# Kernel tuning notes

Hardware: AMD Instinct MI355X
Metric: run time of the kernel (lower is better)

## Reference

```python
import jax, jax.numpy as jnp
import numpy as np

# ---- static config (from init_kwargs) ----
B_, L_, DM = 4, 2048, 1024
EXPAND, HEADDIM, DSTATE, DCONV = 2, 64, 64, 7
DIN = EXPAND * DM            # 2048
NH = DIN // HEADDIM          # 32
CONV_DIM = DIN + 2 * DSTATE  # 2176 (x, B, C go through the depthwise conv)
DPROJ = 2 * DIN + 2 * DSTATE + 2 * NH  # 4288 (z, xBC, dt_fwd, dt_bwd)
EPS = 1e-5


def setup_inputs() -> dict:
    key = jax.random.key(0)
    ks = jax.random.split(key, 8)
    s = lambda d: 1.0 / np.sqrt(d)
    # dt_bias = inv_softplus(dt) with dt ~ logUniform(1e-3, 0.1)  (Mamba2/Hydra init)
    dt = jnp.exp(jax.random.uniform(ks[3], (NH,)) * (np.log(0.1) - np.log(0.001)) + np.log(0.001))
    return {
        "x": jax.random.normal(ks[0], (B_, L_, DM), jnp.float32),
        "ln_gamma": jnp.ones((DM,), jnp.float32),
        "ln_beta": jnp.zeros((DM,), jnp.float32),
        "W_in": jax.random.normal(ks[1], (DPROJ, DM), jnp.float32) * s(DM),
        "conv_w": jax.random.normal(ks[2], (CONV_DIM, DCONV), jnp.float32) * s(DCONV),
        "conv_b": jnp.zeros((CONV_DIM,), jnp.float32),
        "dt_bias": jnp.log(jnp.expm1(dt)),
        "A_log": jnp.log(jax.random.uniform(ks[4], (NH,), minval=1.0, maxval=16.0)),
        "fc_D_w": jax.random.normal(ks[5], (NH, DIN), jnp.float32) * s(DIN),
        "D": jnp.ones((NH,), jnp.float32),
        "norm_w": jnp.ones((DIN,), jnp.float32),
        "W_out": jax.random.normal(ks[6], (DM, DIN), jnp.float32) * s(DIN),
    }


def _hydra_layer(x, ln_gamma, ln_beta, W_in, conv_w, conv_b, dt_bias, A_log,
                 fc_D_w, D, norm_w, W_out):
    res = x
    # LayerNorm
    mu = jnp.mean(x, -1, keepdims=True)
    var = jnp.mean((x - mu) ** 2, -1, keepdims=True)
    u = (x - mu) * jax.lax.rsqrt(var + EPS) * ln_gamma + ln_beta

    # input projection -> z (gate), xBC (conv stream), dt (fwd+bwd)
    zxbcdt = jnp.einsum('bld,pd->blp', u, W_in)
    z = zxbcdt[..., :DIN]
    xBC = zxbcdt[..., DIN:DIN + CONV_DIM]
    dt = zxbcdt[..., DIN + CONV_DIM:]               # (B,L,2*NH)

    # depthwise 'same' conv along L + SiLU (bidirectional model -> symmetric pad)
    xBC_c = jax.lax.conv_general_dilated(
        xBC.transpose(0, 2, 1), conv_w[:, None, :], (1,),
        [(DCONV // 2, DCONV // 2)], feature_group_count=CONV_DIM)
    xBC = jax.nn.silu((xBC_c + conv_b[None, :, None]).transpose(0, 2, 1))

    xs = xBC[..., :DIN]                             # (B,L,DIN)
    Bm = xBC[..., DIN:DIN + DSTATE]                 # (B,L,N)
    Cm = xBC[..., DIN + DSTATE:]                    # (B,L,N)

    flip = lambda a: a[:, ::-1]
    # stack forward and (flipped) backward direction along batch
    dt2 = jax.nn.softplus(jnp.concatenate([dt[..., :NH], flip(dt[..., NH:])], 0) + dt_bias)  # (2B,L,NH)
    x2 = jnp.concatenate([xs, flip(xs)], 0).reshape(2 * B_, L_, NH, HEADDIM)
    B2 = jnp.concatenate([Bm, flip(Bm)], 0)
    C2 = jnp.concatenate([Cm, flip(Cm)], 0)

    A = -jnp.exp(A_log)                             # (NH,)
    dA = jnp.exp(dt2 * A)                           # (2B,L,NH)

    # selective SSM recurrence: h_t = dA_t * h_{t-1} + dt_t * x_t B_t^T ; y_t = h_t C_t
    def step(h, inp):
        dA_t, dt_t, B_t, C_t, x_t = inp
        dBx = (dt_t[:, :, None, None] * x_t[..., None]) * B_t[:, None, None, :]
        h = dA_t[:, :, None, None] * h + dBx        # (2B,NH,P,N)
        y = jnp.einsum('bhpn,bn->bhp', h, C_t)
        return h, y

    h0 = jnp.zeros((2 * B_, NH, HEADDIM, DSTATE), x.dtype)
    tr = lambda a: jnp.moveaxis(a, 1, 0)
    _, ys = jax.lax.scan(step, h0, (tr(dA), tr(dt2), tr(B2), tr(C2), tr(x2)))
    y = jnp.moveaxis(ys, 0, 1)                      # (2B,L,NH,P)

    # shift by one: strictly off-diagonal part of the quasiseparable mixing matrix
    y = jnp.concatenate([jnp.zeros_like(y[:, :1]), y[:, :-1]], axis=1)
    y = y[:B_] + flip(y[B_:])                       # (B,L,NH,P)

    # data-dependent diagonal: D(x) = fc_D(x) + D, applied per head
    Ddata = jnp.einsum('bld,hd->blh', xs, fc_D_w) + D
    y = y + xs.reshape(B_, L_, NH, HEADDIM) * Ddata[..., None]
    y = y.reshape(B_, L_, DIN)

    # gated RMSNorm (norm after gate)
    y = y * jax.nn.silu(z)
    y = y * jax.lax.rsqrt(jnp.mean(y * y, -1, keepdims=True) + EPS) * norm_w

    # out proj + residual (dropout is identity in eval)
    return res + jnp.einsum('bli,di->bld', y, W_out)


def reference(x, ln_gamma, ln_beta, W_in, conv_w, conv_b, dt_bias, A_log,
              fc_D_w, D, norm_w, W_out):
    return _hydra_layer(x, ln_gamma, ln_beta, W_in, conv_w, conv_b, dt_bias,
                        A_log, fc_D_w, D, norm_w, W_out)
```

## Files before the change

kernel.cpp:

```cpp
#include <hip/hip_runtime.h>
#include <stdint.h>

#define B_   4
#define L_   2048
#define DM   1024
#define DIN  2048
#define NH   32
#define HD   64
#define DSTATE 64
#define DCONV  7
#define CONV_DIM 2176
#define DPROJ 4288
#define NPAD 4352
#define BL   8192
#define EPS  1e-5f
#define QC   128
#define NCH  16

typedef unsigned short u16;
typedef unsigned int   u32;
typedef __bf16 bf16x8 __attribute__((ext_vector_type(8)));
typedef float  f32x4  __attribute__((ext_vector_type(4)));

__device__ __forceinline__ float b2f(u32 b) { return __uint_as_float(b << 16); }
__device__ __forceinline__ u16 f2b(float f) {
    u32 u = __float_as_uint(f);
    u32 r = (u + 0x7fffu + ((u >> 16) & 1u)) >> 16;
    return (u16)r;
}
__device__ __forceinline__ void unpack8(uint4 v, float* f) {
    f[0] = b2f(v.x & 0xffffu); f[1] = b2f(v.x >> 16);
    f[2] = b2f(v.y & 0xffffu); f[3] = b2f(v.y >> 16);
    f[4] = b2f(v.z & 0xffffu); f[5] = b2f(v.z >> 16);
    f[6] = b2f(v.w & 0xffffu); f[7] = b2f(v.w >> 16);
}
__device__ __forceinline__ uint4 pack8(const float* f) {
    uint4 v;
    v.x = (u32)f2b(f[0]) | ((u32)f2b(f[1]) << 16);
    v.y = (u32)f2b(f[2]) | ((u32)f2b(f[3]) << 16);
    v.z = (u32)f2b(f[4]) | ((u32)f2b(f[5]) << 16);
    v.w = (u32)f2b(f[6]) | ((u32)f2b(f[7]) << 16);
    return v;
}
__device__ __forceinline__ int xts(int p, int s) { return p * 136 + ((p >> 3) << 3) + s; }
__device__ __forceinline__ void gload_lds16(const u16* g, u16* l) {
    __builtin_amdgcn_global_load_lds((const __attribute__((address_space(1))) void*)g,
                                     (__attribute__((address_space(3))) void*)l, 16, 0, 0);
}

__global__ __launch_bounds__(256) void k_cvt_win(const float* __restrict__ W, u16* __restrict__ Wb) {
    int idx = blockIdx.x * 256 + threadIdx.x;
    int n = idx >> 10;
    float v = (n < DPROJ) ? W[(size_t)n * DM + (idx & 1023)] : 0.f;
    Wb[idx] = f2b(v);
}
__global__ __launch_bounds__(256) void k_cvt_wout(const float* __restrict__ W, u16* __restrict__ Wb) {
    int idx = blockIdx.x * 256 + threadIdx.x;
    Wb[idx] = f2b(W[idx]);
}
__global__ __launch_bounds__(256) void k_cvt_fcd(const float* __restrict__ W, u16* __restrict__ Wb) {
    int idx = blockIdx.x * 256 + threadIdx.x;
    Wb[idx] = f2b(W[idx]);
}

__global__ __launch_bounds__(256) void k_ln(const float* __restrict__ x, const float* __restrict__ g,
                                            const float* __restrict__ be, u16* __restrict__ u) {
    int row = blockIdx.x, tid = threadIdx.x;
    const float4* xr = (const float4*)(x + (size_t)row * DM);
    float4 v = xr[tid];
    float s1 = v.x + v.y + v.z + v.w;
    float s2 = v.x * v.x + v.y * v.y + v.z * v.z + v.w * v.w;
    for (int o = 32; o; o >>= 1) { s1 += __shfl_down(s1, o); s2 += __shfl_down(s2, o); }
    __shared__ float ls1[4], ls2[4];
    int w = tid >> 6;
    if ((tid & 63) == 0) { ls1[w] = s1; ls2[w] = s2; }
    __syncthreads();
    float t1 = ls1[0] + ls1[1] + ls1[2] + ls1[3];
    float t2 = ls2[0] + ls2[1] + ls2[2] + ls2[3];
    float mu = t1 * (1.f / DM);
    float var = t2 * (1.f / DM) - mu * mu;
    float rs = rsqrtf(var + EPS);
    float4 gv = ((const float4*)g)[tid];
    float4 bv = ((const float4*)be)[tid];
    float o0 = (v.x - mu) * rs * gv.x + bv.x;
    float o1 = (v.y - mu) * rs * gv.y + bv.y;
    float o2 = (v.z - mu) * rs * gv.z + bv.z;
    float o3 = (v.w - mu) * rs * gv.w + bv.w;
    uint2 p;
    p.x = (u32)f2b(o0) | ((u32)f2b(o1) << 16);
    p.y = (u32)f2b(o2) | ((u32)f2b(o3) << 16);
    ((uint2*)(u + (size_t)row * DM))[tid] = p;
}

#define G3_DSA(d, kh, ms)                                                        \
  { _Pragma("unroll")                                                            \
    for (int mi = 0; mi < 4; mi++)                                               \
      af_[mi] = *(const bf16x8*)&Asl[d][kh][a_rd + (ms) * 2048 + mi * 512]; }
#define G3_DSB(d, kh)                                                            \
  { _Pragma("unroll")                                                            \
    for (int nj = 0; nj < 4; nj++)                                               \
      bf_[nj] = *(const bf16x8*)&Bsl[d][kh][b_rd + nj * 512]; }
#define G3_STA(d, kh, tau)                                                       \
  { const size_t ko = (size_t)((tau) * 64 + (kh) * 32);                          \
    gload_lds16(Ag + a_src + ko, &Asl[d][kh][st_l]);                             \
    gload_lds16(Ag + a_src + srowK + ko, &Asl[d][kh][st_l + 512]); }
#define G3_STB(d, kh, tau)                                                       \
  { const size_t ko = (size_t)((tau) * 64 + (kh) * 32);                          \
    gload_lds16(Bg + b_src + ko, &Bsl[d][kh][st_l]);                             \
    gload_lds16(Bg + b_src + srowK + ko, &Bsl[d][kh][st_l + 512]); }
#define G3_MM(ms)                                                                \
  { __builtin_amdgcn_s_barrier();                                                \
    asm volatile("s_waitcnt lgkmcnt(0)" ::: "memory");                           \
    __builtin_amdgcn_sched_barrier(0);                                           \
    __builtin_amdgcn_s_setprio(1);                                               \
    _Pragma("unroll")                                                            \
    for (int mi = 0; mi < 4; mi++)                                               \
      _Pragma("unroll")                                                          \
      for (int nj = 0; nj < 4; nj++)                                             \
        acc[ms][mi][nj] = __builtin_amdgcn_mfma_f32_16x16x32_bf16(af_[mi], bf_[nj], acc[ms][mi][nj], 0, 0, 0); \
    __builtin_amdgcn_s_setprio(0);                                               \
    asm volatile("" ::: "memory");                                               \
    __builtin_amdgcn_s_barrier(); }
#define G3_VM4 asm volatile("s_waitcnt vmcnt(4)" ::: "memory");
#define G3_VM0 asm volatile("s_waitcnt vmcnt(0)" ::: "memory");

__global__ __launch_bounds__(512, 2) void k_gemm256(const u16* __restrict__ Ag, const u16* __restrict__ Bg,
                                                    int K, u16* __restrict__ obf, int ldo) {
    __shared__ __align__(16) u16 Asl[2][2][8192];
    __shared__ __align__(16) u16 Bsl[2][2][8192];
    const int tid = threadIdx.x;
    const int w = tid >> 6, lane = tid & 63, lr = lane & 15, lq = lane >> 4;
    const int wm = w >> 2, wn = w & 3;
    const int bid = blockIdx.x;
    const int swz = (bid & 7) * 68 + (bid >> 3);
    const int bx = swz >> 5, by = swz & 31;
    const int m0 = by * 256, n0 = bx * 256;
    const int sr = lane >> 2;
    const int sc = (lane & 3) ^ ((lane >> 3) & 3);
    const size_t a_src = (size_t)(m0 + w * 32 + sr) * K + sc * 8;
    const size_t b_src = (size_t)(n0 + w * 32 + sr) * K + sc * 8;
    const size_t srowK = (size_t)16 * K;
    const int st_l = w * 1024;
    const int swc = (lq ^ ((lr >> 1) & 3)) << 3;
    const int a_rd = (wm * 128 + lr) * 32 + swc;
    const int b_rd = (wn * 64 + lr) * 32 + swc;

    f32x4 acc[2][4][4];
    #pragma unroll
    for (int s = 0; s < 2; s++)
        #pragma unroll
        for (int i = 0; i < 4; i++)
            #pragma unroll
            for (int j = 0; j < 4; j++) acc[s][i][j] = (f32x4){0.f, 0.f, 0.f, 0.f};

    bf16x8 af_[4], bf_[4];

    G3_STA(0, 0, 0); G3_STB(0, 0, 0);
    G3_STA(0, 1, 0); G3_STB(0, 1, 0);
    G3_STA(1, 0, 1); G3_STB(1, 0, 1);
    G3_VM0;
    __builtin_amdgcn_s_barrier();

    const int NI = K >> 7;
    for (int i = 0; i < NI - 1; ++i) {
        const int t = 2 * i;
        G3_DSB(0, 0) G3_DSA(0, 0, 0) G3_STA(1, 1, t + 1);          G3_MM(0)
        G3_DSA(0, 0, 1) G3_STB(1, 1, t + 1); G3_VM4;               G3_MM(1)
        G3_DSB(0, 1) G3_DSA(0, 1, 0) G3_STA(0, 0, t + 2);          G3_MM(0)
        G3_DSA(0, 1, 1) G3_STB(0, 0, t + 2);                       G3_MM(1)
        G3_DSB(1, 0) G3_DSA(1, 0, 0) G3_STA(0, 1, t + 2);          G3_MM(0)
        G3_DSA(1, 0, 1) G3_STB(0, 1, t + 2); G3_VM4;               G3_MM(1)
        G3_DSB(1, 1) G3_DSA(1, 1, 0) G3_STA(1, 0, t + 3);          G3_MM(0)
        G3_DSA(1, 1, 1) G3_STB(1, 0, t + 3);                       G3_MM(1)
    }
    {
        const int t = 2 * (NI - 1);
        G3_DSB(0, 0) G3_DSA(0, 0, 0) G3_STA(1, 1, t + 1);          G3_MM(0)
        G3_DSA(0, 0, 1) G3_STB(1, 1, t + 1); G3_VM4;               G3_MM(1)
        G3_DSB(0, 1) G3_DSA(0, 1, 0)                               G3_MM(0)
        G3_DSA(0, 1, 1)                                            G3_MM(1)
        G3_DSB(1, 0) G3_DSA(1, 0, 0)                               G3_MM(0)
        G3_DSA(1, 0, 1) G3_VM0;                                    G3_MM(1)
        G3_DSB(1, 1) G3_DSA(1, 1, 0)                               G3_MM(0)
        G3_DSA(1, 1, 1)                                            G3_MM(1)
    }

    #pragma unroll
    for (int ms = 0; ms < 2; ms++)
        #pragma unroll
        for (int mi = 0; mi < 4; mi++)
            #pragma unroll
            for (int nj = 0; nj < 4; nj++)
                #pragma unroll
                for (int rr = 0; rr < 4; rr++) {
                    int m = m0 + wm * 128 + ms * 64 + mi * 16 + lq * 4 + rr;
                    int n = n0 + wn * 64 + nj * 16 + lr;
                    obf[(size_t)m * ldo + n] = f2b(acc[ms][mi][nj][rr]);
                }
}

__global__ __launch_bounds__(256) void k_gemm_bt(const u16* __restrict__ A, const u16* __restrict__ Bw,
                                                 int M, int N, int K, int out_bf16,
                                                 u16* __restrict__ obf, int ldo,
                                                 float* __restrict__ ofp, const float* __restrict__ res) {
    __shared__ __align__(16) u16 As[128 * 64];
    __shared__ __align__(16) u16 Bs[128 * 64];
    int tid = threadIdx.x;
    int m0 = blockIdx.y * 128, n0 = blockIdx.x * 128;
    int w = tid >> 6, lane = tid & 63;
    int wm = (w >> 1) * 64, wn = (w & 1) * 64;
    int lr = lane & 15, lq = lane >> 4;

    f32x4 acc[4][4];
    #pragma unroll
    for (int i = 0; i < 4; i++)
        #pragma unroll
        for (int j = 0; j < 4; j++) acc[i][j] = (f32x4){0.f, 0.f, 0.f, 0.f};

    for (int kt = 0; kt < K; kt += 64) {
        #pragma unroll
        for (int it = 0; it < 4; it++) {
            int s_idx = it * 256 + tid;
            int row = s_idx >> 3;
            int kcg = (s_idx & 7) ^ (row & 7);
            u16* lbase_a = &As[(it * 256 + w * 64) * 8];
            u16* lbase_b = &Bs[(it * 256 + w * 64) * 8];
            gload_lds16(A + (size_t)(m0 + row) * K + kt + kcg * 8, lbase_a);
            gload_lds16(Bw + (size_t)(n0 + row) * K + kt + kcg * 8, lbase_b);
        }
        __syncthreads();
        #pragma unroll
        for (int kk = 0; kk < 2; kk++) {
            bf16x8 af[4], bfr[4];
            #pragma unroll
            for (int i = 0; i < 4; i++) {
                int row = wm + 16 * i + lr;
                af[i] = *(const bf16x8*)&As[row * 64 + (((kk * 4 + lq)) ^ (row & 7)) * 8];
            }
            #pragma unroll
            for (int j = 0; j < 4; j++) {
                int row = wn + 16 * j + lr;
                bfr[j] = *(const bf16x8*)&Bs[row * 64 + (((kk * 4 + lq)) ^ (row & 7)) * 8];
            }
            #pragma unroll
            for (int i = 0; i < 4; i++)
                #pragma unroll
                for (int j = 0; j < 4; j++)
                    acc[i][j] = __builtin_amdgcn_mfma_f32_16x16x32_bf16(af[i], bfr[j], acc[i][j], 0, 0, 0);
        }
        __syncthreads();
    }
    #pragma unroll
    for (int i = 0; i < 4; i++) {
        #pragma unroll
        for (int j = 0; j < 4; j++) {
            #pragma unroll
            for (int rr = 0; rr < 4; rr++) {
                int m = m0 + wm + 16 * i + lq * 4 + rr;
                int n = n0 + wn + 16 * j + lr;
                float v = acc[i][j][rr];
                if (out_bf16) obf[(size_t)m * ldo + n] = f2b(v);
                else          ofp[(size_t)m * ldo + n] = v + res[(size_t)m * ldo + n];
            }
        }
    }
}

__global__ __launch_bounds__(256) void k_dproj(const u16* __restrict__ xs, const u16* __restrict__ fcb,
                                               const float* __restrict__ Dv, float* __restrict__ Dd) {
    __shared__ __align__(16) u16 As[32 * 72];
    __shared__ __align__(16) u16 Bs[32 * 72];
    int tid = threadIdx.x;
    int m0 = blockIdx.x * 32;
    int w = tid >> 6, lane = tid & 63, lr = lane & 15, lq = lane >> 4;
    int mt = (w & 1) * 16, nt = (w >> 1) * 16;
    int r = tid >> 3, kc = tid & 7;
    f32x4 acc = (f32x4){0.f, 0.f, 0.f, 0.f};
    for (int kt = 0; kt < DIN; kt += 64) {
        *(uint4*)&As[r * 72 + kc * 8] = *(const uint4*)(xs + (size_t)(m0 + r) * DIN + kt + kc * 8);
        *(uint4*)&Bs[r * 72 + kc * 8] = *(const uint4*)(fcb + (size_t)r * DIN + kt + kc * 8);
        __syncthreads();
        #pragma unroll
        for (int ks = 0; ks < 2; ks++) {
            bf16x8 a = *(const bf16x8*)&As[(mt + lr) * 72 + ks * 32 + lq * 8];
            bf16x8 b = *(const bf16x8*)&Bs[(nt + lr) * 72 + ks * 32 + lq * 8];
            acc = __builtin_amdgcn_mfma_f32_16x16x32_bf16(a, b, acc, 0, 0, 0);
        }
        __syncthreads();
    }
    #pragma unroll
    for (int rr = 0; rr < 4; rr++) {
        int m = m0 + mt + lq * 4 + rr;
        int n = nt + lr;
        Dd[(size_t)m * 32 + n] = acc[rr] + Dv[n];
    }
}

__global__ __launch_bounds__(256) void k_conv(const u16* __restrict__ zx, const float* __restrict__ cw,
                                              const float* __restrict__ cb, u16* __restrict__ xs,
                                              u16* __restrict__ BCb) {
    __shared__ u16 sh[262 * 64];
    int c0 = blockIdx.x * 64, t0 = blockIdx.y * 256, b = blockIdx.z;
    int tid = threadIdx.x;
    int c = tid & 63, tg = tid >> 6;
    for (int it = 0; it < 66; it++) {
        int r = it * 4 + tg;
        if (r < 262) {
            int t = t0 + r - 3;
            u16 v = 0;
            if (t >= 0 && t < L_) v = zx[(size_t)(b * L_ + t) * NPAD + DIN + c0 + c];
            sh[r * 64 + c] = v;
        }
    }
    float wgt[7];
    #pragma unroll
    for (int k = 0; k < 7; k++) wgt[k] = cw[(c0 + c) * 7 + k];
    float bias = cb[c0 + c];
    __syncthreads();
    int cg = c0 + c;
    for (int tt = 0; tt < 64; tt++) {
        int tl = tt * 4 + tg;
        float a = bias;
        #pragma unroll
        for (int k = 0; k < 7; k++) a += b2f(sh[(tl + k) * 64 + c]) * wgt[k];
        float v = a / (1.f + __expf(-a));
        size_t row = (size_t)b * L_ + (t0 + tl);
        if (cg < DIN) xs[row * DIN + cg] = f2b(v);
        else          BCb[row * 128 + (cg - DIN)] = f2b(v);
    }
}

__global__ __launch_bounds__(256) void k_chunk(const u16* __restrict__ xs, const u16* __restrict__ BCb,
                                               const u16* __restrict__ zx, const float* __restrict__ dt_bias,
                                               const float* __restrict__ A_log, u16* __restrict__ y0,
                                               u16* __restrict__ y1, float* __restrict__ wout,
                                               float* __restrict__ decay, u16* __restrict__ scb) {
    __shared__ __align__(16) u16 ab[18432];
    __shared__ __align__(16) u16 XT[8768];
    __shared__ __align__(16) u16 BT[8768];
    __shared__ __align__(16) float dts_s[128];
    __shared__ __align__(16) float lda_s[128];
    __shared__ __align__(16) float wend[128];
    __shared__ __align__(16) double cumd[128];

    const int blk = blockIdx.x;
    const int c = blk & 15, dbh = blk >> 4;
    const int h = dbh & 31, b = (dbh >> 5) & 3, dir = dbh >> 7;
    const int tid = threadIdx.x, w = tid >> 6, lane = tid & 63, lr = lane & 15, lq = lane >> 4;
    const int s0 = c * QC;
    u16* yo = dir ? y1 : y0;

    if (tid < 128) {
        int s = s0 + tid;
        int t = dir ? (L_ - 1 - s) : s;
        float draw = b2f(zx[(size_t)(b * L_ + t) * NPAD + (DIN + CONV_DIM) + dir * 32 + h]);
        float xb = draw + dt_bias[h];
        float dt2 = (xb > 20.f) ? xb : log1pf(__expf(xb));
        dts_s[tid] = dt2;
        lda_s[tid] = -__expf(A_log[h]) * dt2;
    }
    {
        int sl0 = tid >> 3, ng = (tid & 7) * 8;
        #pragma unroll
        for (int it = 0; it < 4; it++) {
            int sl = sl0 + it * 32;
            int s = s0 + sl;
            int t = dir ? (L_ - 1 - s) : s;
            size_t row = (size_t)b * L_ + t;
            const u16* bcr = BCb + row * 128;
            uint4 cv = *(const uint4*)(bcr + 64 + ng);
            *(uint4*)&ab[sl * 72 + ng] = cv;
            uint4 pb = *(const uint4*)(bcr + ng);
            *(uint4*)&ab[9216 + sl * 72 + ng] = pb;
            u16 bh[8] = {(u16)(pb.x & 0xffffu), (u16)(pb.x >> 16), (u16)(pb.y & 0xffffu), (u16)(pb.y >> 16),
                         (u16)(pb.z & 0xffffu), (u16)(pb.z >> 16), (u16)(pb.w & 0xffffu), (u16)(pb.w >> 16)};
            #pragma unroll
            for (int i = 0; i < 8; i++) BT[(ng + i) * 136 + ng + sl] = bh[i];
            uint4 xv = *(const uint4*)(xs + row * DIN + h * 64 + ng);
            u16 xh[8] = {(u16)(xv.x & 0xffffu), (u16)(xv.x >> 16), (u16)(xv.y & 0xffffu), (u16)(xv.y >> 16),
                         (u16)(xv.z & 0xffffu), (u16)(xv.z >> 16), (u16)(xv.w & 0xffffu), (u16)(xv.w >> 16)};
            #pragma unroll
            for (int i = 0; i < 8; i++) XT[(ng + i) * 136 + ng + sl] = xh[i];
        }
    }
    __syncthreads();
    if (w == 0) {
        double v0 = (double)lda_s[lane];
        double v1 = (double)lda_s[64 + lane];
        #pragma unroll
        for (int o = 1; o < 64; o <<= 1) {
            double t0 = __shfl_up(v0, o);
            double t1 = __shfl_up(v1, o);
            if (lane >= o) { v0 += t0; v1 += t1; }
        }
        double tot0 = __shfl(v0, 63);
        cumd[lane] = v0;
        cumd[64 + lane] = tot0 + v1;
    }
    bf16x8 af[2][2];
    #pragma unroll
    for (int ti = 0; ti < 2; ti++)
        #pragma unroll
        for (int ks = 0; ks < 2; ks++)
            af[ti][ks] = *(const bf16x8*)&ab[(w * 32 + ti * 16 + lr) * 72 + ks * 32 + lq * 8];
    f32x4 accg[2][8];
    #pragma unroll
    for (int ti = 0; ti < 2; ti++)
        #pragma unroll
        for (int si = 0; si < 8; si++) accg[ti][si] = (f32x4){0.f, 0.f, 0.f, 0.f};
    #pragma unroll
    for (int si = 0; si < 8; si++)
        #pragma unroll
        for (int ks = 0; ks < 2; ks++) {
            bf16x8 bf = *(const bf16x8*)&ab[9216 + (si * 16 + lr) * 72 + ks * 32 + lq * 8];
            accg[0][si] = __builtin_amdgcn_mfma_f32_16x16x32_bf16(af[0][ks], bf, accg[0][si], 0, 0, 0);
            accg[1][si] = __builtin_amdgcn_mfma_f32_16x16x32_bf16(af[1][ks], bf, accg[1][si], 0, 0, 0);
        }
    __syncthreads();
    if (tid < 128) wend[tid] = __expf((float)(cumd[127] - cumd[tid])) * dts_s[tid];
    {
        double cumt_d[8];
        #pragma unroll
        for (int ti = 0; ti < 2; ti++)
            #pragma unroll
            for (int r = 0; r < 4; r++) cumt_d[ti * 4 + r] = cumd[w * 32 + ti * 16 + lq * 4 + r];
        double cums_d[8]; float dts_l[8];
        #pragma unroll
        for (int si = 0; si < 8; si++) { cums_d[si] = cumd[si * 16 + lr]; dts_l[si] = dts_s[si * 16 + lr]; }
        #pragma unroll
        for (int ti = 0; ti < 2; ti++)
            #pragma unroll
            for (int si = 0; si < 8; si++)
                #pragma unroll
                for (int r = 0; r < 4; r++) {
                    int t_l = w * 32 + ti * 16 + lq * 4 + r;
                    int s_l = si * 16 + lr;
                    float v = 0.f;
                    if (s_l <= t_l)
                        v = __expf((float)(cumt_d[ti * 4 + r] - cums_d[si])) * dts_l[si] * accg[ti][si][r];
                    ab[xts(t_l, s_l)] = f2b(v);
                }
    }
    __syncthreads();
    f32x4 acc[2][4];
    #pragma unroll
    for (int ti = 0; ti < 2; ti++)
        #pragma unroll
        for (int pj = 0; pj < 4; pj++) acc[ti][pj] = (f32x4){0.f, 0.f, 0.f, 0.f};
    #pragma unroll
    for (int ks = 0; ks < 4; ks++) {
        bf16x8 a0 = *(const bf16x8*)&ab[xts(w * 32 + lr, ks * 32 + lq * 8)];
        bf16x8 a1 = *(const bf16x8*)&ab[xts(w * 32 + 16 + lr, ks * 32 + lq * 8)];
        #pragma unroll
        for (int pj = 0; pj < 4; pj++) {
            bf16x8 bf = *(const bf16x8*)&XT[xts(pj * 16 + lr, ks * 32 + lq * 8)];
            acc[0][pj] = __builtin_amdgcn_mfma_f32_16x16x32_bf16(a0, bf, acc[0][pj], 0, 0, 0);
            acc[1][pj] = __builtin_amdgcn_mfma_f32_16x16x32_bf16(a1, bf, acc[1][pj], 0, 0, 0);
        }
    }
    #pragma unroll
    for (int ti = 0; ti < 2; ti++)
        #pragma unroll
        for (int pj = 0; pj < 4; pj++)
            #pragma unroll
            for (int r = 0; r < 4; r++) {
                int t_l = w * 32 + ti * 16 + lq * 4 + r;
                int s = s0 + t_l;
                int t = dir ? (L_ - 1 - s) : s;
                yo[((size_t)b * L_ + t) * DIN + h * 64 + pj * 16 + lr] = f2b(acc[ti][pj][r]);
            }
    f32x4 accs[4];
    #pragma unroll
    for (int nj = 0; nj < 4; nj++) accs[nj] = (f32x4){0.f, 0.f, 0.f, 0.f};
    #pragma unroll
    for (int ks = 0; ks < 4; ks++) {
        uint4 xv = *(const uint4*)&XT[xts(w * 16 + lr, ks * 32 + lq * 8)];
        float xf[8]; unpack8(xv, xf);
        float4 w0 = *(const float4*)&wend[ks * 32 + lq * 8];
        float4 w1 = *(const float4*)&wend[ks * 32 + lq * 8 + 4];
        float fs[8] = {xf[0]*w0.x, xf[1]*w0.y, xf[2]*w0.z, xf[3]*w0.w,
                       xf[4]*w1.x, xf[5]*w1.y, xf[6]*w1.z, xf[7]*w1.w};
        bf16x8 a = __builtin_bit_cast(bf16x8, pack8(fs));
        #pragma unroll
        for (int nj = 0; nj < 4; nj++) {
            bf16x8 bb = *(const bf16x8*)&BT[xts(nj * 16 + lr, ks * 32 + lq * 8)];
            accs[nj] = __builtin_amdgcn_mfma_f32_16x16x32_bf16(a, bb, accs[nj], 0, 0, 0);
        }
    }
    #pragma unroll
    for (int nj = 0; nj < 4; nj++)
        #pragma unroll
        for (int r = 0; r < 4; r++) {
            int p = w * 16 + lq * 4 + r, n = nj * 16 + lr;
            scb[(size_t)blk * 4096 + p * 64 + n] = f2b(accs[nj][r]);
        }
    if (tid < 128) wout[dbh * 2048 + s0 + tid] = __expf((float)cumd[tid]);
    if (tid == 0)  decay[blk] = __expf((float)cumd[127]);
}

__global__ __launch_bounds__(256) void k_hscan(const float* __restrict__ decay, u16* __restrict__ scb) {
    int dbh = blockIdx.x, tid = threadIdx.x;
    u16* base = scb + (size_t)dbh * 16 * 4096 + tid * 16;
    float hcur[16];
    #pragma unroll
    for (int i = 0; i < 16; i++) hcur[i] = 0.f;
    for (int c = 0; c < NCH; c++) {
        u16* sg = base + (size_t)c * 4096;
        uint4 q0 = *(const uint4*)sg;
        uint4 q1 = *(const uint4*)(sg + 8);
        float sf[16]; unpack8(q0, sf); unpack8(q1, sf + 8);
        *(uint4*)sg       = pack8(hcur);
        *(uint4*)(sg + 8) = pack8(hcur + 8);
        float dk = decay[dbh * 16 + c];
        #pragma unroll
        for (int i = 0; i < 16; i++) hcur[i] = dk * hcur[i] + sf[i];
    }
}

__global__ __launch_bounds__(256) void k_inter(const u16* __restrict__ BCb, const float* __restrict__ wout,
                                               const u16* __restrict__ hin, u16* __restrict__ y0,
                                               u16* __restrict__ y1) {
    __shared__ __align__(16) u16 Csc[128 * 72];
    __shared__ __align__(16) u16 hs[64 * 72];
    const int blk = blockIdx.x;
    const int c = blk & 15, dbh = blk >> 4;
    const int h = dbh & 31, b = (dbh >> 5) & 3, dir = dbh >> 7;
    const int tid = threadIdx.x, w = tid >> 6, lane = tid & 63, lr = lane & 15, lq = lane >> 4;
    u16* yo = dir ? y1 : y0;

    {
        int g = tid * 16, p = g >> 6, n = g & 63;
        const u16* hg = hin + (size_t)blk * 4096 + g;
        *(uint4*)&hs[p * 72 + n]     = *(const uint4*)hg;
        *(uint4*)&hs[p * 72 + n + 8] = *(const uint4*)(hg + 8);
    }
    const int sl0 = tid >> 3, ng = (tid & 7) * 8;
    #pragma unroll
    for (int it = 0; it < 4; it++) {
        int sl = sl0 + it * 32;
        int s = c * QC + sl;
        int t = dir ? (L_ - 1 - s) : s;
        const u16* bcr = BCb + ((size_t)b * L_ + t) * 128 + 64 + ng;
        float sc = wout[dbh * 2048 + s];
        uint4 cv = *(const uint4*)bcr;
        float cf[8]; unpack8(cv, cf);
        float f[8] = {cf[0]*sc, cf[1]*sc, cf[2]*sc, cf[3]*sc, cf[4]*sc, cf[5]*sc, cf[6]*sc, cf[7]*sc};
        *(uint4*)&Csc[sl * 72 + ng] = pack8(f);
    }
    __syncthreads();
    f32x4 acc[2][4];
    #pragma unroll
    for (int ti = 0; ti < 2; ti++)
        #pragma unroll
        for (int pj = 0; pj < 4; pj++) acc[ti][pj] = (f32x4){0.f, 0.f, 0.f, 0.f};
    #pragma unroll
    for (int ks = 0; ks < 2; ks++) {
        bf16x8 a0 = *(const bf16x8*)&Csc[(w * 32 + lr) * 72 + ks * 32 + lq * 8];
        bf16x8 a1 = *(const bf16x8*)&Csc[(w * 32 + 16 + lr) * 72 + ks * 32 + lq * 8];
        #pragma unroll
        for (int pj = 0; pj < 4; pj++) {
            bf16x8 bb = *(const bf16x8*)&hs[(pj * 16 + lr) * 72 + ks * 32 + lq * 8];
            acc[0][pj] = __builtin_amdgcn_mfma_f32_16x16x32_bf16(a0, bb, acc[0][pj], 0, 0, 0);
            acc[1][pj] = __builtin_amdgcn_mfma_f32_16x16x32_bf16(a1, bb, acc[1][pj], 0, 0, 0);
        }
    }
    #pragma unroll
    for (int ti = 0; ti < 2; ti++)
        #pragma unroll
        for (int pj = 0; pj < 4; pj++)
            #pragma unroll
            for (int r = 0; r < 4; r++) {
                int t_l = w * 32 + ti * 16 + lq * 4 + r;
                int s = c * QC + t_l;
                int t = dir ? (L_ - 1 - s) : s;
                u16* yp = yo + ((size_t)b * L_ + t) * DIN + h * 64 + pj * 16 + lr;
                *yp = f2b(acc[ti][pj][r] + b2f(*yp));
            }
}

__global__ __launch_bounds__(256) void k_gate(const u16* __restrict__ xs, const u16* __restrict__ zx,
                                              const u16* __restrict__ y0, const u16* __restrict__ y1,
                                              const float* __restrict__ Dd,
                                              const float* __restrict__ nw, u16* __restrict__ yn) {
    int row = blockIdx.x, tid = threadIdx.x;
    int t = row & (L_ - 1);
    __shared__ float red[4];
    size_t base = (size_t)row * DIN;
    uint4 xv = ((const uint4*)(xs + base))[tid];
    uint4 zv = ((const uint4*)(zx + (size_t)row * NPAD))[tid];
    uint4 zero4 = {0u, 0u, 0u, 0u};
    uint4 a0 = (t > 0)      ? ((const uint4*)(y0 + base - DIN))[tid] : zero4;
    uint4 a1 = (t < L_ - 1) ? ((const uint4*)(y1 + base + DIN))[tid] : zero4;
    float sD = Dd[(size_t)row * 32 + (tid >> 3)];
    float xf[8], zf[8], f0[8], f1[8];
    unpack8(xv, xf); unpack8(zv, zf); unpack8(a0, f0); unpack8(a1, f1);
    int d0 = tid * 8;
    float g[8]; float ss = 0.f;
    #pragma unroll
    for (int i = 0; i < 8; i++) {
        float yv = f0[i] + f1[i] + xf[i] * sD;
        float z = zf[i];
        float gg = yv * (z / (1.f + __expf(-z)));
        g[i] = gg; ss += gg * gg;
    }
    for (int o = 32; o; o >>= 1) ss += __shfl_down(ss, o);
    if ((tid & 63) == 0) red[tid >> 6] = ss;
    __syncthreads();
    float tot = red[0] + red[1] + red[2] + red[3];
    float r = rsqrtf(tot * (1.f / DIN) + EPS);
    float o8[8];
    #pragma unroll
    for (int i = 0; i < 8; i++) o8[i] = g[i] * r * nw[d0 + i];
    ((uint4*)(yn + base))[tid] = pack8(o8);
}

#define OFF_U     ((size_t)0)
#define OFF_WIN   ((size_t)16777216)
#define OFF_WOUT  ((size_t)25690112)
#define OFF_ZX    ((size_t)29884416)
#define OFF_XS    ((size_t)101187584)
#define OFF_BC    ((size_t)134742016)
#define OFF_DTA   ((size_t)138936320)
#define OFF_Y0    ((size_t)143130624)
#define OFF_Y1    ((size_t)176685056)
#define OFF_YN    ((size_t)210239488)
#define OFF_WO2   OFF_U
#define OFF_DEC   (OFF_U + 2097152)
#define OFF_FCB   (OFF_U + 2113536)
#define OFF_DD    (OFF_U + 2244608)
#define OFF_SCB   OFF_YN

extern "C" void kernel_launch(void* const* d_in, const int* in_sizes, int n_in,
                              void* d_out, int out_size, void* d_ws, size_t ws_size,
                              hipStream_t stream) {
    const float* x       = (const float*)d_in[0];
    const float* ln_g    = (const float*)d_in[1];
    const float* ln_b    = (const float*)d_in[2];
    const float* W_in    = (const float*)d_in[3];
    const float* conv_w  = (const float*)d_in[4];
    const float* conv_b  = (const float*)d_in[5];
    const float* dt_bias = (const float*)d_in[6];
    const float* A_log   = (const float*)d_in[7];
    const float* fc_D_w  = (const float*)d_in[8];
    const float* Dv      = (const float*)d_in[9];
    const float* norm_w  = (const float*)d_in[10];
    const float* W_out   = (const float*)d_in[11];

    char* ws = (char*)d_ws;
    u16*   u_bf  = (u16*)(ws + OFF_U);
    u16*   winb  = (u16*)(ws + OFF_WIN);
    u16*   woutb = (u16*)(ws + OFF_WOUT);
    u16*   zx    = (u16*)(ws + OFF_ZX);
    u16*   xs    = (u16*)(ws + OFF_XS);
    u16*   BCb   = (u16*)(ws + OFF_BC);
    u16*   y0b   = (u16*)(ws + OFF_Y0);
    u16*   y1b   = (u16*)(ws + OFF_Y1);
    u16*   ynb   = (u16*)(ws + OFF_YN);
    float* wo2   = (float*)(ws + OFF_WO2);
    float* dec   = (float*)(ws + OFF_DEC);
    u16*   fcb   = (u16*)(ws + OFF_FCB);
    float* Dd    = (float*)(ws + OFF_DD);
    u16*   scb   = (u16*)(ws + OFF_SCB);

    k_cvt_win <<<(NPAD * DM) / 256, 256, 0, stream>>>(W_in, winb);
    k_cvt_wout<<<(DM * DIN) / 256, 256, 0, stream>>>(W_out, woutb);
    k_ln      <<<BL, 256, 0, stream>>>(x, ln_g, ln_b, u_bf);
    k_gemm256 <<<(NPAD / 256) * (BL / 256), 512, 0, stream>>>(u_bf, winb, DM, zx, NPAD);
    k_cvt_fcd <<<(NH * DIN) / 256, 256, 0, stream>>>(fc_D_w, fcb);
    k_conv    <<<dim3(CONV_DIM / 64, L_ / 256, B_), 256, 0, stream>>>(zx, conv_w, conv_b, xs, BCb);
    k_dproj   <<<BL / 32, 256, 0, stream>>>(xs, fcb, Dv, Dd);
    k_chunk   <<<4096, 256, 0, stream>>>(xs, BCb, zx, dt_bias, A_log, y0b, y1b, wo2, dec, scb);
    k_hscan   <<<256, 256, 0, stream>>>(dec, scb);
    k_inter   <<<4096, 256, 0, stream>>>(BCb, wo2, scb, y0b, y1b);
    k_gate    <<<BL, 256, 0, stream>>>(xs, zx, y0b, y1b, Dd, norm_w, ynb);
    k_gemm_bt <<<dim3(DM / 128, BL / 128), 256, 0, stream>>>(ynb, woutb, BL, DM, DIN, 0, nullptr, DM, (float*)d_out, x);
}
```

Measured before the change: 546.0 us.

## Deepen GEMM global-to-LDS prefetch pipeline with finer vmcnt waits

Restructures the k_gemm256 main loop so B-tile loads are issued one half-step earlier, keeping more global->LDS loads in flight (vmcnt 10 instead of 4). The vmcnt waits move to the end of each MFMA phase, ahead of the barrier, and gain a sched_barrier so they stay in place. The tail uses graded waits (8, 4, 0). The aim is to hide global-memory latency behind the MFMA work, at the risk of LDS buffer reuse hazards if the ordering is wrong.

```diff
diff --git a/kernel.cpp b/kernel.cpp
--- a/kernel.cpp
+++ b/kernel.cpp
@@ -108,8 +108,8 @@
   { const size_t ko = (size_t)((tau) * 64 + (kh) * 32);                          \
     gload_lds16(Bg + b_src + ko, &Bsl[d][kh][st_l]);                             \
     gload_lds16(Bg + b_src + srowK + ko, &Bsl[d][kh][st_l + 512]); }
-#define G3_MM(ms)                                                                \
-  { __builtin_amdgcn_s_barrier();                                                \
+#define G3_CORE(ms)                                                              \
+    __builtin_amdgcn_s_barrier();                                                \
     asm volatile("s_waitcnt lgkmcnt(0)" ::: "memory");                           \
     __builtin_amdgcn_sched_barrier(0);                                           \
     __builtin_amdgcn_s_setprio(1);                                               \
@@ -119,10 +119,16 @@
       for (int nj = 0; nj < 4; nj++)                                             \
         acc[ms][mi][nj] = __builtin_amdgcn_mfma_f32_16x16x32_bf16(af_[mi], bf_[nj], acc[ms][mi][nj], 0, 0, 0); \
     __builtin_amdgcn_s_setprio(0);                                               \
-    asm volatile("" ::: "memory");                                               \
-    __builtin_amdgcn_s_barrier(); }
-#define G3_VM4 asm volatile("s_waitcnt vmcnt(4)" ::: "memory");
-#define G3_VM0 asm volatile("s_waitcnt vmcnt(0)" ::: "memory");
+    __builtin_amdgcn_sched_barrier(0);
+#define G3_MMO(ms)                                                               \
+  { G3_CORE(ms)                                                                  \
+    __builtin_amdgcn_s_barrier();                                                \
+    asm volatile("" ::: "memory"); }
+#define G3_MME(ms, VM)                                                           \
+  { G3_CORE(ms)                                                                  \
+    asm volatile("s_waitcnt vmcnt(" #VM ")" ::: "memory");                       \
+    __builtin_amdgcn_s_barrier();                                                \
+    asm volatile("" ::: "memory"); }
 
 __global__ __launch_bounds__(512, 2) void k_gemm256(const u16* __restrict__ Ag, const u16* __restrict__ Bg,
                                                     int K, u16* __restrict__ obf, int ldo) {
@@ -156,33 +162,35 @@
     bf16x8 af_[4], bf_[4];
 
     G3_STA(0, 0, 0); G3_STB(0, 0, 0);
-    G3_STA(0, 1, 0); G3_STB(0, 1, 0);
-    G3_STA(1, 0, 1); G3_STB(1, 0, 1);
-    G3_VM0;
+    G3_STB(0, 1, 0); G3_STA(0, 1, 0);
+    G3_STB(1, 0, 1); G3_STA(1, 0, 1);
+    G3_STB(1, 1, 1);
+    asm volatile("s_waitcnt vmcnt(10)" ::: "memory");
     __builtin_amdgcn_s_barrier();
+    asm volatile("" ::: "memory");
 
     const int NI = K >> 7;
     for (int i = 0; i < NI - 1; ++i) {
         const int t = 2 * i;
-        G3_DSB(0, 0) G3_DSA(0, 0, 0) G3_STA(1, 1, t + 1);          G3_MM(0)
-        G3_DSA(0, 0, 1) G3_STB(1, 1, t + 1); G3_VM4;               G3_MM(1)
-        G3_DSB(0, 1) G3_DSA(0, 1, 0) G3_STA(0, 0, t + 2);          G3_MM(0)
-        G3_DSA(0, 1, 1) G3_STB(0, 0, t + 2);                       G3_MM(1)
-        G3_DSB(1, 0) G3_DSA(1, 0, 0) G3_STA(0, 1, t + 2);          G3_MM(0)
-        G3_DSA(1, 0, 1) G3_STB(0, 1, t + 2); G3_VM4;               G3_MM(1)
-        G3_DSB(1, 1) G3_DSA(1, 1, 0) G3_STA(1, 0, t + 3);          G3_MM(0)
-        G3_DSA(1, 1, 1) G3_STB(1, 0, t + 3);                       G3_MM(1)
+        G3_DSB(0, 0) G3_DSA(0, 0, 0) G3_STA(1, 1, t + 1);  G3_MMO(0)
+        G3_DSA(0, 0, 1) G3_STB(0, 0, t + 2);               G3_MME(1, 10)
+        G3_DSB(0, 1) G3_DSA(0, 1, 0) G3_STA(0, 0, t + 2);  G3_MMO(0)
+        G3_DSA(0, 1, 1) G3_STB(0, 1, t + 2);               G3_MME(1, 10)
+        G3_DSB(1, 0) G3_DSA(1, 0, 0) G3_STA(0, 1, t + 2);  G3_MMO(0)
+        G3_DSA(1, 0, 1) G3_STB(1, 0, t + 3);               G3_MME(1, 10)
+        G3_DSB(1, 1) G3_DSA(1, 1, 0) G3_STA(1, 0, t + 3);  G3_MMO(0)
+        G3_DSA(1, 1, 1) G3_STB(1, 1, t + 3);               G3_MME(1, 10)
     }
     {
         const int t = 2 * (NI - 1);
-        G3_DSB(0, 0) G3_DSA(0, 0, 0) G3_STA(1, 1, t + 1);          G3_MM(0)
-        G3_DSA(0, 0, 1) G3_STB(1, 1, t + 1); G3_VM4;               G3_MM(1)
-        G3_DSB(0, 1) G3_DSA(0, 1, 0)                               G3_MM(0)
-        G3_DSA(0, 1, 1)                                            G3_MM(1)
-        G3_DSB(1, 0) G3_DSA(1, 0, 0)                               G3_MM(0)
-        G3_DSA(1, 0, 1) G3_VM0;                                    G3_MM(1)
-        G3_DSB(1, 1) G3_DSA(1, 1, 0)                               G3_MM(0)
-        G3_DSA(1, 1, 1)                                            G3_MM(1)
+        G3_DSB(0, 0) G3_DSA(0, 0, 0) G3_STA(1, 1, t + 1);  G3_MMO(0)
+        G3_DSA(0, 0, 1);                                   G3_MME(1, 8)
+        G3_DSB(0, 1) G3_DSA(0, 1, 0);                      G3_MMO(0)
+        G3_DSA(0, 1, 1);                                   G3_MME(1, 4)
+        G3_DSB(1, 0) G3_DSA(1, 0, 0);                      G3_MMO(0)
+        G3_DSA(1, 0, 1);                                   G3_MME(1, 0)
+        G3_DSB(1, 1) G3_DSA(1, 1, 0);                      G3_MMO(0)
+        G3_DSA(1, 1, 1);                                   G3_MMO(1)
     }
 
     #pragma unroll
```

New measurement: 535.3 us. Within noise of the previous version (-1.9%).
